# Kernel optimization log

Hardware: AMD Instinct MI355X
Metric: run time of the kernel (lower is better)

Reference implementation:

```python
import jax, jax.numpy as jnp
import numpy as np
from jax import lax


def setup_inputs() -> dict:
    key = jax.random.key(0)
    k1, k2 = jax.random.split(key)
    B, L1, L2, D = 128, 512, 512, 16
    s1_batch = jax.random.normal(k1, (B, L1, D), dtype=jnp.float32)
    s2_batch = jax.random.normal(k2, (B, L2, D), dtype=jnp.float32)
    return {"s1_batch": s1_batch, "s2_batch": s2_batch}


def _pairwise_sq_dists(s1, s2):
    # C[b,i,j] = sum_d (s1[b,i,d] - s2[b,j,d])^2, computed without a [B,L1,L2,D] temp
    s1sq = jnp.sum(s1 * s1, axis=-1)  # [B, L1]
    s2sq = jnp.sum(s2 * s2, axis=-1)  # [B, L2]
    cross = jnp.einsum("bid,bjd->bij", s1, s2)  # [B, L1, L2]
    return s1sq[:, :, None] + s2sq[:, None, :] - 2.0 * cross


def _dtw_final(C):
    # C: [B, L1, L2] cost matrix; returns DTW[:, -1, -1] via row-wise scan
    # Row 0: DTW[0, j] = cumsum of costs (only left moves allowed)
    row0 = jnp.cumsum(C[:, 0, :], axis=1)  # [B, L2]

    def row_step(prev_row, c_row):
        # prev_row, c_row: [B, L2]
        first = c_row[:, 0] + prev_row[:, 0]  # j = 0: only 'up' predecessor
        cs = c_row[:, 1:].T      # [L2-1, B]
        ups = prev_row[:, 1:].T  # DTW[i-1, j]
        dgs = prev_row[:, :-1].T # DTW[i-1, j-1]

        def col_step(left, xs):
            c_j, up, dg = xs
            val = c_j + jnp.minimum(left, jnp.minimum(up, dg))
            return val, val

        _, rest = lax.scan(col_step, first, (cs, ups, dgs))  # rest: [L2-1, B]
        new_row = jnp.concatenate([first[:, None], rest.T], axis=1)
        return new_row, None

    final_row, _ = lax.scan(row_step, row0, jnp.moveaxis(C[:, 1:, :], 1, 0))
    return final_row[:, -1]  # [B]


def reference(s1_batch, s2_batch):
    C = _pairwise_sq_dists(s1_batch, s2_batch)
    dtw_end = _dtw_final(C)
    return jnp.mean(jnp.sqrt(dtw_end))
```

## Files before the change

kernel.cpp:

```cpp
#include <hip/hip_runtime.h>
#include <math.h>


#define TL 512
#define TD 16
#define TNB 128
#define BIGF 3.0e38f
#define INFF __builtin_inff()
#define XSTR 20
#define WOFF 71
#define EP 8
#define NE 99

typedef float f32x2 __attribute__((ext_vector_type(2)));
typedef float f32x4 __attribute__((ext_vector_type(4)));

__device__ inline f32x2 pk_fma(f32x2 a, f32x2 b, f32x2 c) {
    f32x2 d;
    asm("v_pk_fma_f32 %0, %1, %2, %3" : "=v"(d) : "v"(a), "v"(b), "v"(c));
    return d;
}
__device__ inline f32x2 pk_mul(f32x2 a, f32x2 b) {
    f32x2 d;
    asm("v_pk_mul_f32 %0, %1, %2" : "=v"(d) : "v"(a), "v"(b));
    return d;
}
__device__ inline float min3f(float a, float b, float c) {
    float d;
    asm("v_min3_f32 %0, %1, %2, %3" : "=v"(d) : "v"(a), "v"(b), "v"(c));
    return d;
}
template<int CTRL, int RM, bool BC>
__device__ inline float dpp_mov(float old_, float src) {
    return __int_as_float(__builtin_amdgcn_update_dpp(
        __float_as_int(old_), __float_as_int(src), CTRL, RM, 0xf, BC));
}

struct XR { f32x4 q0, q1, q2, q3; float sq; };

__device__ inline void xissue(unsigned base, int r, XR& x) {
    int rc = r < 0 ? 0 : (r > TL - 1 ? TL - 1 : r);
    unsigned a = base + (unsigned)(rc * (XSTR * 4));
    asm volatile("ds_read_b128 %0, %1 offset:0"  : "=v"(x.q0) : "v"(a));
    asm volatile("ds_read_b128 %0, %1 offset:16" : "=v"(x.q1) : "v"(a));
    asm volatile("ds_read_b128 %0, %1 offset:32" : "=v"(x.q2) : "v"(a));
    asm volatile("ds_read_b128 %0, %1 offset:48" : "=v"(x.q3) : "v"(a));
    asm volatile("ds_read_b32  %0, %1 offset:64" : "=v"(x.sq) : "v"(a));
}

#define WAITC() { asm volatile("s_waitcnt lgkmcnt(10)" ::: "memory"); \
                  __builtin_amdgcn_sched_barrier(0); }

__device__ inline void sub(const XR& x, int r,
                           const f32x2 (&y0)[8], const f32x2 (&y1)[8],
                           f32x2 ys0, f32x2 ys1,
                           float& pv0, float& pv1, float& o1,
                           float bL, float bD, bool lane0) {
    const f32x2* xd = (const f32x2*)&x;
    f32x2 a0 = ys0, a1 = ys1;
    #pragma unroll
    for (int k = 0; k < 8; ++k) {
        a0 = pk_fma(xd[k], y0[k], a0);
        a1 = pk_fma(xd[k], y1[k], a1);
    }
    const float c0 = x.sq + (a0.x + a0.y);
    const float c1 = x.sq + (a1.x + a1.y);

    float left = dpp_mov<0x138, 0xf, false>(BIGF, pv1);
    float diag = dpp_mov<0x138, 0xf, false>(BIGF, o1);
    if (lane0) { left = bL; diag = bD; }
    o1 = pv1;

    const float v0 = c0 + min3f(pv0, left, diag);
    const float v1 = c1 + min3f(pv1, v0, pv0);
    const bool valid = (unsigned)r < (unsigned)TL;
    pv0 = valid ? v0 : pv0;
    pv1 = valid ? v1 : pv1;
}

__global__ __launch_bounds__(256, 1) void dtw_split_kernel(const float* __restrict__ s1,
                                                           const float* __restrict__ s2,
                                                           float* __restrict__ ws) {
    const int b   = blockIdx.x;
    const int tid = threadIdx.x;
    const int W   = tid >> 6;
    const int l   = tid & 63;

    __shared__ float xlds[TL * XSTR];
    __shared__ f32x4 pkt[2][4][2];

    const float* s1b = s1 + (size_t)b * TL * TD;

    #pragma unroll
    for (int q = 0; q < 2; ++q) {
        const int r = 2 * tid + q;
        const f32x4* src = (const f32x4*)(s1b + r * TD);
        f32x4 q0 = src[0], q1 = src[1], q2 = src[2], q3 = src[3];
        f32x4* dst = (f32x4*)(xlds + r * XSTR);
        dst[0] = q0; dst[1] = q1; dst[2] = q2; dst[3] = q3;
        f32x2 a_ = pk_mul(f32x2{q0.x, q0.y}, f32x2{q0.x, q0.y});
        a_ = pk_fma(f32x2{q0.z, q0.w}, f32x2{q0.z, q0.w}, a_);
        a_ = pk_fma(f32x2{q1.x, q1.y}, f32x2{q1.x, q1.y}, a_);
        a_ = pk_fma(f32x2{q1.z, q1.w}, f32x2{q1.z, q1.w}, a_);
        a_ = pk_fma(f32x2{q2.x, q2.y}, f32x2{q2.x, q2.y}, a_);
        a_ = pk_fma(f32x2{q2.z, q2.w}, f32x2{q2.z, q2.w}, a_);
        a_ = pk_fma(f32x2{q3.x, q3.y}, f32x2{q3.x, q3.y}, a_);
        a_ = pk_fma(f32x2{q3.z, q3.w}, f32x2{q3.z, q3.w}, a_);
        xlds[r * XSTR + 16] = a_.x + a_.y;
    }
    if (tid < 64) ((float*)pkt)[tid] = BIGF;

    const int j0 = 2 * (64 * W + l);
    f32x2 y0[8], y1[8];
    const float* yp0 = s2 + ((size_t)b * TL + j0) * TD;
    #pragma unroll
    for (int k = 0; k < 8; ++k) {
        y0[k] = *(const f32x2*)(yp0 + 2 * k);
        y1[k] = *(const f32x2*)(yp0 + TD + 2 * k);
    }
    f32x2 s0a = pk_mul(y0[0], y0[0]), s1a = pk_mul(y1[0], y1[0]);
    #pragma unroll
    for (int k = 1; k < 8; ++k) {
        s0a = pk_fma(y0[k], y0[k], s0a);
        s1a = pk_fma(y1[k], y1[k], s1a);
    }
    const f32x2 ys0 = {s0a.x + s0a.y, 0.f};
    const f32x2 ys1 = {s1a.x + s1a.y, 0.f};
    #pragma unroll
    for (int k = 0; k < 8; ++k) {
        y0[k] = pk_mul(y0[k], f32x2{-2.f, -2.f});
        y1[k] = pk_mul(y1[k], f32x2{-2.f, -2.f});
    }

    __syncthreads();

    const unsigned base = (unsigned)(uintptr_t)&xlds[0];
    const int gL = WOFF * W + l;
    const bool lane0 = (l == 0);
    float pv0 = INFF, pv1 = INFF, o1 = INFF;
    float carry = (W == 0) ? 0.f : BIGF;

    XR x0, x1, x2, x3;
    xissue(base, 0 - gL, x0);
    xissue(base, 1 - gL, x1);
    xissue(base, 2 - gL, x2);

    for (int e = 0; e < NE; ++e) {
        float lb0 = BIGF, lb1 = BIGF, lb2 = BIGF, lb3 = BIGF;
        float lb4 = BIGF, lb5 = BIGF, lb6 = BIGF, lb7 = BIGF;
        if (W > 0) {
            f32x4 pA = pkt[(e + 1) & 1][W - 1][0];
            f32x4 pB = pkt[(e + 1) & 1][W - 1][1];
            lb0 = pA.x; lb1 = pA.y; lb2 = pA.z; lb3 = pA.w;
            lb4 = pB.x; lb5 = pB.y; lb6 = pB.z; lb7 = pB.w;
        }
        const int rb = EP * e - gL;
        float t0, t1, t2, t3, t4, t5, t6, t7;

        WAITC(); xissue(base, rb + 3,  x3);
        sub(x0, rb + 0, y0, y1, ys0, ys1, pv0, pv1, o1, lb0, carry, lane0); t0 = pv1;
        WAITC(); xissue(base, rb + 4,  x0);
        sub(x1, rb + 1, y0, y1, ys0, ys1, pv0, pv1, o1, lb1, lb0, lane0);   t1 = pv1;
        WAITC(); xissue(base, rb + 5,  x1);
        sub(x2, rb + 2, y0, y1, ys0, ys1, pv0, pv1, o1, lb2, lb1, lane0);   t2 = pv1;
        WAITC(); xissue(base, rb + 6,  x2);
        sub(x3, rb + 3, y0, y1, ys0, ys1, pv0, pv1, o1, lb3, lb2, lane0);   t3 = pv1;
        WAITC(); xissue(base, rb + 7,  x3);
        sub(x0, rb + 4, y0, y1, ys0, ys1, pv0, pv1, o1, lb4, lb3, lane0);   t4 = pv1;
        WAITC(); xissue(base, rb + 8,  x0);
        sub(x1, rb + 5, y0, y1, ys0, ys1, pv0, pv1, o1, lb5, lb4, lane0);   t5 = pv1;
        WAITC(); xissue(base, rb + 9,  x1);
        sub(x2, rb + 6, y0, y1, ys0, ys1, pv0, pv1, o1, lb6, lb5, lane0);   t6 = pv1;
        WAITC(); xissue(base, rb + 10, x2);
        sub(x3, rb + 7, y0, y1, ys0, ys1, pv0, pv1, o1, lb7, lb6, lane0);   t7 = pv1;

        carry = lb7;

        if (l == 63 && W < 3) {
            pkt[e & 1][W][0] = f32x4{t0, t1, t2, t3};
            pkt[e & 1][W][1] = f32x4{t4, t5, t6, t7};
        }
        __syncthreads();
    }

    if (W == 3 && l == 63) ws[b] = sqrtf(pv1);
}

__global__ void dtw_reduce_kernel(const float* __restrict__ ws, float* __restrict__ out) {
    const int t = threadIdx.x;
    float v = ws[t] + ws[t + 64];
    #pragma unroll
    for (int d2 = 32; d2 > 0; d2 >>= 1) v += __shfl_down(v, d2);
    if (t == 0) out[0] = v * (1.0f / TNB);
}

extern "C" void kernel_launch(void* const* d_in, const int* in_sizes, int n_in,
                              void* d_out, int out_size, void* d_ws, size_t ws_size,
                              hipStream_t stream) {
    const float* s1 = (const float*)d_in[0];
    const float* s2 = (const float*)d_in[1];
    float* ws  = (float*)d_ws;
    float* out = (float*)d_out;

    dtw_split_kernel<<<TNB, 256, 0, stream>>>(s1, s2, ws);
    dtw_reduce_kernel<<<1, 64, 0, stream>>>(ws, out);
}
```

Before: 96.01 us.

## Shift s1 rows across lanes with DPP instead of per-lane LDS reads

Each lane now keeps its s1 row in registers, and each step it takes the previous lane's row through a DPP row shift. Only lane 0 of each wave takes the new row from a broadcast LDS read at the wave's row offset. Every lane in a wave reads the same LDS address, which is meant to turn many distinct-address LDS reads into broadcasts and cut LDS bandwidth pressure. The cost is 17 extra DPP moves per step on the dependent path. There is also a risk at lane boundaries within the 16-lane DPP rows, because row_shr with bound_ctrl off keeps the old value (the LDS row) only at the row edge, and lanes 16, 32 and 48 need the correct neighbour.

```diff
diff --git a/kernel.cpp b/kernel.cpp
--- a/kernel.cpp
+++ b/kernel.cpp
@@ -30,15 +30,14 @@
     asm("v_min3_f32 %0, %1, %2, %3" : "=v"(d) : "v"(a), "v"(b), "v"(c));
     return d;
 }
-template<int CTRL, int RM, bool BC>
-__device__ inline float dpp_mov(float old_, float src) {
+__device__ inline float dsh(float old_, float src) {
     return __int_as_float(__builtin_amdgcn_update_dpp(
-        __float_as_int(old_), __float_as_int(src), CTRL, RM, 0xf, BC));
-}
-
-struct XR { f32x4 q0, q1, q2, q3; float sq; };
-
-__device__ inline void xissue(unsigned base, int r, XR& x) {
+        __float_as_int(old_), __float_as_int(src), 0x138, 0xf, 0xf, false));
+}
+
+struct XF { f32x4 q0, q1, q2, q3; float sq; };
+
+__device__ inline void fissue(unsigned base, int r, XF& x) {
     int rc = r < 0 ? 0 : (r > TL - 1 ? TL - 1 : r);
     unsigned a = base + (unsigned)(rc * (XSTR * 4));
     asm volatile("ds_read_b128 %0, %1 offset:0"  : "=v"(x.q0) : "v"(a));
@@ -51,23 +50,34 @@
 #define WAITC() { asm volatile("s_waitcnt lgkmcnt(10)" ::: "memory"); \
                   __builtin_amdgcn_sched_barrier(0); }
 
-__device__ inline void sub(const XR& x, int r,
+__device__ inline void xshift(const XF& f, f32x2 (&X)[8], float& Xsq) {
+    X[0].x = dsh(f.q0.x, X[0].x); X[0].y = dsh(f.q0.y, X[0].y);
+    X[1].x = dsh(f.q0.z, X[1].x); X[1].y = dsh(f.q0.w, X[1].y);
+    X[2].x = dsh(f.q1.x, X[2].x); X[2].y = dsh(f.q1.y, X[2].y);
+    X[3].x = dsh(f.q1.z, X[3].x); X[3].y = dsh(f.q1.w, X[3].y);
+    X[4].x = dsh(f.q2.x, X[4].x); X[4].y = dsh(f.q2.y, X[4].y);
+    X[5].x = dsh(f.q2.z, X[5].x); X[5].y = dsh(f.q2.w, X[5].y);
+    X[6].x = dsh(f.q3.x, X[6].x); X[6].y = dsh(f.q3.y, X[6].y);
+    X[7].x = dsh(f.q3.z, X[7].x); X[7].y = dsh(f.q3.w, X[7].y);
+    Xsq    = dsh(f.sq,   Xsq);
+}
+
+__device__ inline void sub(const f32x2 (&X)[8], float Xsq, int r,
                            const f32x2 (&y0)[8], const f32x2 (&y1)[8],
                            f32x2 ys0, f32x2 ys1,
                            float& pv0, float& pv1, float& o1,
                            float bL, float bD, bool lane0) {
-    const f32x2* xd = (const f32x2*)&x;
     f32x2 a0 = ys0, a1 = ys1;
     #pragma unroll
     for (int k = 0; k < 8; ++k) {
-        a0 = pk_fma(xd[k], y0[k], a0);
-        a1 = pk_fma(xd[k], y1[k], a1);
-    }
-    const float c0 = x.sq + (a0.x + a0.y);
-    const float c1 = x.sq + (a1.x + a1.y);
-
-    float left = dpp_mov<0x138, 0xf, false>(BIGF, pv1);
-    float diag = dpp_mov<0x138, 0xf, false>(BIGF, o1);
+        a0 = pk_fma(X[k], y0[k], a0);
+        a1 = pk_fma(X[k], y1[k], a1);
+    }
+    const float c0 = Xsq + (a0.x + a0.y);
+    const float c1 = Xsq + (a1.x + a1.y);
+
+    float left = dsh(BIGF, pv1);
+    float diag = dsh(BIGF, o1);
     if (lane0) { left = bL; diag = bD; }
     o1 = pv1;
 
@@ -136,14 +146,18 @@
 
     const unsigned base = (unsigned)(uintptr_t)&xlds[0];
     const int gL = WOFF * W + l;
+    const int rw = -WOFF * W;
     const bool lane0 = (l == 0);
     float pv0 = INFF, pv1 = INFF, o1 = INFF;
     float carry = (W == 0) ? 0.f : BIGF;
 
-    XR x0, x1, x2, x3;
-    xissue(base, 0 - gL, x0);
-    xissue(base, 1 - gL, x1);
-    xissue(base, 2 - gL, x2);
+    f32x2 X[8] = {};
+    float Xsq = 0.f;
+
+    XF f0, f1, f2, f3;
+    fissue(base, rw + 0, f0);
+    fissue(base, rw + 1, f1);
+    fissue(base, rw + 2, f2);
 
     for (int e = 0; e < NE; ++e) {
         float lb0 = BIGF, lb1 = BIGF, lb2 = BIGF, lb3 = BIGF;
@@ -154,25 +168,26 @@
             lb0 = pA.x; lb1 = pA.y; lb2 = pA.z; lb3 = pA.w;
             lb4 = pB.x; lb5 = pB.y; lb6 = pB.z; lb7 = pB.w;
         }
-        const int rb = EP * e - gL;
+        const int rb  = EP * e - gL;
+        const int rl0 = EP * e + rw;
         float t0, t1, t2, t3, t4, t5, t6, t7;
 
-        WAITC(); xissue(base, rb + 3,  x3);
-        sub(x0, rb + 0, y0, y1, ys0, ys1, pv0, pv1, o1, lb0, carry, lane0); t0 = pv1;
-        WAITC(); xissue(base, rb + 4,  x0);
-        sub(x1, rb + 1, y0, y1, ys0, ys1, pv0, pv1, o1, lb1, lb0, lane0);   t1 = pv1;
-        WAITC(); xissue(base, rb + 5,  x1);
-        sub(x2, rb + 2, y0, y1, ys0, ys1, pv0, pv1, o1, lb2, lb1, lane0);   t2 = pv1;
-        WAITC(); xissue(base, rb + 6,  x2);
-        sub(x3, rb + 3, y0, y1, ys0, ys1, pv0, pv1, o1, lb3, lb2, lane0);   t3 = pv1;
-        WAITC(); xissue(base, rb + 7,  x3);
-        sub(x0, rb + 4, y0, y1, ys0, ys1, pv0, pv1, o1, lb4, lb3, lane0);   t4 = pv1;
-        WAITC(); xissue(base, rb + 8,  x0);
-        sub(x1, rb + 5, y0, y1, ys0, ys1, pv0, pv1, o1, lb5, lb4, lane0);   t5 = pv1;
-        WAITC(); xissue(base, rb + 9,  x1);
-        sub(x2, rb + 6, y0, y1, ys0, ys1, pv0, pv1, o1, lb6, lb5, lane0);   t6 = pv1;
-        WAITC(); xissue(base, rb + 10, x2);
-        sub(x3, rb + 7, y0, y1, ys0, ys1, pv0, pv1, o1, lb7, lb6, lane0);   t7 = pv1;
+        WAITC(); xshift(f0, X, Xsq); fissue(base, rl0 + 3,  f3);
+        sub(X, Xsq, rb + 0, y0, y1, ys0, ys1, pv0, pv1, o1, lb0, carry, lane0); t0 = pv1;
+        WAITC(); xshift(f1, X, Xsq); fissue(base, rl0 + 4,  f0);
+        sub(X, Xsq, rb + 1, y0, y1, ys0, ys1, pv0, pv1, o1, lb1, lb0, lane0);   t1 = pv1;
+        WAITC(); xshift(f2, X, Xsq); fissue(base, rl0 + 5,  f1);
+        sub(X, Xsq, rb + 2, y0, y1, ys0, ys1, pv0, pv1, o1, lb2, lb1, lane0);   t2 = pv1;
+        WAITC(); xshift(f3, X, Xsq); fissue(base, rl0 + 6,  f2);
+        sub(X, Xsq, rb + 3, y0, y1, ys0, ys1, pv0, pv1, o1, lb3, lb2, lane0);   t3 = pv1;
+        WAITC(); xshift(f0, X, Xsq); fissue(base, rl0 + 7,  f3);
+        sub(X, Xsq, rb + 4, y0, y1, ys0, ys1, pv0, pv1, o1, lb4, lb3, lane0);   t4 = pv1;
+        WAITC(); xshift(f1, X, Xsq); fissue(base, rl0 + 8,  f0);
+        sub(X, Xsq, rb + 5, y0, y1, ys0, ys1, pv0, pv1, o1, lb5, lb4, lane0);   t5 = pv1;
+        WAITC(); xshift(f2, X, Xsq); fissue(base, rl0 + 9,  f1);
+        sub(X, Xsq, rb + 6, y0, y1, ys0, ys1, pv0, pv1, o1, lb6, lb5, lane0);   t6 = pv1;
+        WAITC(); xshift(f3, X, Xsq); fissue(base, rl0 + 10, f2);
+        sub(X, Xsq, rb + 7, y0, y1, ys0, ys1, pv0, pv1, o1, lb7, lb6, lane0);   t7 = pv1;
 
         carry = lb7;
 
```

Result: slower. 123.8 us (+28.9%).
